# Optimization experiments

Measured on AMD Instinct MI355X. Metric: run time of the kernel, lower is better.

## Reference

```python
import jax, jax.numpy as jnp
import numpy as np

P = 8.0  # Lp norm order for NormDist layers (finite-p distance conv)
CHUNK = 8  # output-channel chunk for memory-bounded distance computation
EPS = 8.0 / 255.0


def lp_norm(d, p=P):
    # stable Lp norm over last axis: m * (sum((d/m)^p))^(1/p)
    m = jnp.max(d, axis=-1)
    ms = jnp.where(m > 0, m, 1.0)
    s = jnp.sum((d / ms[..., None]) ** p, axis=-1)
    ss = jnp.where(m > 0, s, 1.0)
    return m * ss ** (1.0 / p)


def extract_patches(t, k, s, pad):
    # [B,C,H,W] -> [B, L, C*k*k] (torch-unfold channel-major ordering), L=Ho*Wo
    pt = jax.lax.conv_general_dilated_patches(t, (k, k), (s, s), [(pad, pad), (pad, pad)])
    B, F, Ho, Wo = pt.shape
    return pt.reshape(B, F, Ho * Wo).transpose(0, 2, 1), Ho, Wo


def normdist_conv(c, lo, hi, w, k, s, pad):
    # Lp-distance conv with interval bound propagation on (center, lower, upper)
    pc, Ho, Wo = extract_patches(c, k, s, pad)
    pl, _, _ = extract_patches(lo, k, s, pad)
    ph, _, _ = extract_patches(hi, k, s, pad)
    O = w.shape[0]
    wf = w.reshape(O, -1)  # [O, F]

    def per_chunk(wc):  # wc: [CHUNK, F]
        dc = jnp.abs(pc[:, :, None, :] - wc)                     # [B,L,CHUNK,F]
        oc = lp_norm(dc)
        # per-element distance bounds given lo <= x <= hi
        dl = jnp.maximum(jnp.maximum(pl[:, :, None, :] - wc, wc - ph[:, :, None, :]), 0.0)
        ol = lp_norm(dl)
        dh = jnp.maximum(jnp.abs(pl[:, :, None, :] - wc), jnp.abs(ph[:, :, None, :] - wc))
        oh = lp_norm(dh)
        return oc, ol, oh

    oc, ol, oh = jax.lax.map(per_chunk, wf.reshape(O // CHUNK, CHUNK, -1))

    def to_img(t):  # [nch, B, L, CHUNK] -> [B, O, Ho, Wo]
        nch, B, L, ch = t.shape
        return t.transpose(1, 0, 3, 2).reshape(B, nch * ch, Ho, Wo)

    return to_img(oc), to_img(ol), to_img(oh)


def bound_relu(c, lo, hi):
    return jax.nn.relu(c), jax.nn.relu(lo), jax.nn.relu(hi)


def _mp(t):
    return jax.lax.reduce_window(t, -jnp.inf, jax.lax.max, (1, 1, 3, 3), (1, 1, 2, 2), 'VALID')


def bound_maxpool(c, lo, hi):
    return _mp(c), _mp(lo), _mp(hi)


def bound_linear(c, lo, hi, W, b=None):
    oc = c @ W.T
    mid = ((lo + hi) * 0.5) @ W.T
    rad = ((hi - lo) * 0.5) @ jnp.abs(W).T
    if b is not None:
        oc = oc + b
        mid = mid + b
    return oc, mid - rad, mid + rad


def setup_inputs() -> dict:
    key = jax.random.key(0)
    ks = jax.random.split(key, 10)
    x = jax.random.normal(ks[0], (16, 3, 32, 32), jnp.float32)
    lower = x - EPS
    upper = x + EPS
    w1 = jax.random.normal(ks[1], (96, 3, 7, 7), jnp.float32)
    w2 = jax.random.normal(ks[2], (256, 96, 5, 5), jnp.float32)
    w3 = jax.random.normal(ks[3], (384, 256, 3, 3), jnp.float32)
    w4 = jax.random.normal(ks[4], (384, 384, 3, 3), jnp.float32)
    w5 = jax.random.normal(ks[5], (256, 384, 3, 3), jnp.float32)
    fw1 = jax.random.normal(ks[6], (1024, 2304), jnp.float32) * 0.02
    fw2 = jax.random.normal(ks[7], (512, 1024), jnp.float32) * 0.03
    fw3 = jax.random.normal(ks[8], (10, 512), jnp.float32) * 0.04
    fb3 = jax.random.normal(ks[9], (10,), jnp.float32)
    return {"x": x, "lower": lower, "upper": upper, "w1": w1, "w2": w2, "w3": w3,
            "w4": w4, "w5": w5, "fw1": fw1, "fw2": fw2, "fw3": fw3, "fb3": fb3}


def reference(x, lower, upper, w1, w2, w3, w4, w5, fw1, fw2, fw3, fb3):
    c, l, u = normdist_conv(x, lower, upper, w1, 7, 2, 2)   # 32 -> 15
    c, l, u = bound_relu(c, l, u)
    c, l, u = bound_maxpool(c, l, u)                        # 15 -> 7
    c, l, u = normdist_conv(c, l, u, w2, 5, 1, 2)           # 7 -> 7
    c, l, u = bound_relu(c, l, u)
    c, l, u = bound_maxpool(c, l, u)                        # 7 -> 3
    c, l, u = normdist_conv(c, l, u, w3, 3, 1, 1)
    c, l, u = bound_relu(c, l, u)
    c, l, u = normdist_conv(c, l, u, w4, 3, 1, 1)
    c, l, u = bound_relu(c, l, u)
    c, l, u = normdist_conv(c, l, u, w5, 3, 1, 1)
    c, l, u = bound_relu(c, l, u)
    B = c.shape[0]
    c, l, u = c.reshape(B, -1), l.reshape(B, -1), u.reshape(B, -1)
    c, l, u = bound_linear(c, l, u, fw1)
    c, l, u = bound_relu(c, l, u)
    c, l, u = bound_linear(c, l, u, fw2)
    c, l, u = bound_relu(c, l, u)
    c, l, u = bound_linear(c, l, u, fw3, fb3)
    # final negation swaps the roles of lower/upper
    return (-c, -u, -l)
```

## Files before the change

kernel.cpp:

```cpp
#include <hip/hip_runtime.h>
#include <math.h>


__device__ __forceinline__ float rt8(float s) { return sqrtf(sqrtf(sqrtf(s))); }

__device__ __forceinline__ void tap16(float w, float pc, float pl, float pu,
                                      float& aC, float& aL, float& aH)
{
    float a = pc - w; float a2 = a * a, a4 = a2 * a2; aC = fmaf(a4, a4, aC);
    float x = pl - w, y = pu - w;
    float dl = fmaxf(fmaxf(x, -y), 0.f);
    float e2 = dl * dl, e4 = e2 * e2; aL = fmaf(e4, e4, aL);
    float h2 = fmaxf(x * x, y * y);
    float h4 = h2 * h2; aH = fmaf(h4, h4, aH);
}

__launch_bounds__(256)
__global__ void wtrans4(const float* __restrict__ W2, const float* __restrict__ W3,
                        const float* __restrict__ W4, const float* __restrict__ W5,
                        float* __restrict__ T2, float* __restrict__ T3,
                        float* __restrict__ T4, float* __restrict__ T5)
{
    constexpr int nt2 = 4 * 38, nt3 = 6 * 36, nt4 = 6 * 54, nt5 = 4 * 54;
    int bid = blockIdx.x;
    const float* W; float* T; int O, CK, t;
    if (bid < nt2)                   { W = W2; T = T2; O = 256; CK = 2400; t = bid; }
    else if (bid < nt2 + nt3)        { W = W3; T = T3; O = 384; CK = 2304; t = bid - nt2; }
    else if (bid < nt2 + nt3 + nt4)  { W = W4; T = T4; O = 384; CK = 3456; t = bid - nt2 - nt3; }
    else                             { W = W5; T = T5; O = 256; CK = 3456; t = bid - nt2 - nt3 - nt4; }
    int tilesC = (CK + 63) / 64;
    int to = t / tilesC, tc = t - to * tilesC;
    int o0 = to * 64, c0 = tc * 64;
    __shared__ float tile[64][65];
    int lane = threadIdx.x & 63, wv = threadIdx.x >> 6;
    #pragma unroll
    for (int i = 0; i < 16; ++i) {
        int row = wv + i * 4;
        int c = c0 + lane;
        tile[row][lane] = (c < CK) ? W[(size_t)(o0 + row) * CK + c] : 0.f;
    }
    __syncthreads();
    #pragma unroll
    for (int i = 0; i < 16; ++i) {
        int row = wv + i * 4;
        int c = c0 + row;
        if (c < CK) T[(size_t)c * O + o0 + lane] = tile[lane][row];
    }
}

template<int K, int S, int PAD, int CC, int HIN, int WIN, int HO, int WO>
__launch_bounds__(256)
__global__ void conv_a(const float* __restrict__ IC, const float* __restrict__ IL,
                       const float* __restrict__ IU, const float* __restrict__ W,
                       float* __restrict__ OUT, int B, int Cin, int O, int OG)
{
    constexpr int PH = (HO - 1) * S + K;
    constexpr int PW = (WO - 1) * S + K;
    constexpr int PP = PH * PW;
    constexpr int HW = HIN * WIN;
    constexpr int NP = HO * WO;
    constexpr int ROUNDS = (NP + 63) / 64;
    __shared__ float lds[CC * 3 * PP];

    int og = blockIdx.x % OG;
    int b  = (blockIdx.x / OG) % B;
    int tid = threadIdx.x;

    for (int i = tid; i < CC * 3 * PP; i += 256) lds[i] = 0.f;
    __syncthreads();
    for (int tsel = 0; tsel < 3; ++tsel) {
        const float* src = (tsel == 0 ? IC : (tsel == 1 ? IL : IU))
                         + (size_t)b * Cin * HW;
        for (int e = tid; e < CC * HW; e += 256) {
            int c = e / HW, p = e % HW;
            int pr = p / WIN, pw_ = p % WIN;
            lds[c * 3 * PP + tsel * PP + (pr + PAD) * PW + (pw_ + PAD)] = src[e];
        }
    }
    __syncthreads();

    int wave = tid >> 6, lane = tid & 63;
    int o = __builtin_amdgcn_readfirstlane(og * 4 + wave);
    const float* wp = W + (size_t)o * Cin * (K * K);

    for (int r = 0; r < ROUNDS; ++r) {
        int pos = r * 64 + lane;
        bool act = pos < NP;
        int pp = act ? pos : 0;
        int oh = pp / WO, ow = pp % WO;
        const float* sl = lds + (oh * S) * PW + ow * S;
        const float* wc = wp;
        float aC = 0.f, aL = 0.f, aH = 0.f;
        for (int c = 0; c < CC; ++c) {
            #pragma unroll
            for (int kh = 0; kh < K; ++kh)
                #pragma unroll
                for (int kw = 0; kw < K; ++kw) {
                    float w = wc[kh * K + kw];
                    tap16(w, sl[kh * PW + kw], sl[PP + kh * PW + kw],
                          sl[2 * PP + kh * PW + kw], aC, aL, aH);
                }
            sl += 3 * PP; wc += K * K;
        }
        if (act) {
            size_t N = (size_t)B * O * NP;
            size_t oidx = ((size_t)b * O + o) * NP + pos;
            OUT[oidx] = rt8(aC); OUT[N + oidx] = rt8(aL); OUT[2 * N + oidx] = rt8(aH);
        }
    }
}

template<int CC>
__launch_bounds__(256)
__global__ void conv2_kernel(const float* __restrict__ IN, const float* __restrict__ WT,
                             float* __restrict__ P, int nin)
{
    constexpr int B = 16, Cin = 96, O = 256;
    constexpr size_t N = (size_t)B * O * 49;
    __shared__ float slab[CC * 165];
    int x = blockIdx.x;
    int oh   = x % 7;
    int b    = (x / 7) % B;
    int chunk = x / (7 * B);
    int c0 = chunk * CC;
    int tid = threadIdx.x;

    for (int i = tid; i < CC * 165; i += 256) {
        int c = i / 165; int rem = i - c * 165;
        int tsel = rem / 55; int rr = rem - tsel * 55;
        int r = rr / 11, col = rr - r * 11;
        int ih = oh + r - 2, iw = col - 2;
        float v = 0.f;
        if ((unsigned)ih < 7u && (unsigned)iw < 7u)
            v = IN[(size_t)tsel * nin + ((size_t)b * Cin + c0 + c) * 49 + ih * 7 + iw];
        slab[i] = v;
    }
    __syncthreads();

    int o = tid;
    float aC[7], aL[7], aH[7];
    #pragma unroll
    for (int u = 0; u < 7; ++u) { aC[u] = 0.f; aL[u] = 0.f; aH[u] = 0.f; }

    for (int c = 0; c < CC; ++c) {
        const float* wp = WT + (size_t)((c0 + c) * 25) * O + o;
        float w[25];
        #pragma unroll
        for (int t = 0; t < 25; ++t) w[t] = wp[(size_t)t * O];
        const float* sb = slab + c * 165;
        #pragma unroll
        for (int r = 0; r < 5; ++r) {
            #pragma unroll
            for (int i = 0; i < 11; ++i) {
                float xc = sb[r * 11 + i];
                float xl = sb[55 + r * 11 + i];
                float xu = sb[110 + r * 11 + i];
                #pragma unroll
                for (int ow = 0; ow < 7; ++ow) {
                    int kw = i - ow;
                    if (kw >= 0 && kw < 5)
                        tap16(w[r * 5 + kw], xc, xl, xu, aC[ow], aL[ow], aH[ow]);
                }
            }
        }
    }

    float* Pc = P + (size_t)chunk * 3 * N;
    size_t rowbase = ((size_t)(b * 7 + oh) * 7) * O + o;
    #pragma unroll
    for (int u = 0; u < 7; ++u) {
        Pc[rowbase + (size_t)u * O]         = aC[u];
        Pc[N + rowbase + (size_t)u * O]     = aL[u];
        Pc[2 * N + rowbase + (size_t)u * O] = aH[u];
    }
}

__global__ void conv2_combine(const float* __restrict__ P, float* __restrict__ OUT, int NCH)
{
    constexpr int B = 16, O = 256;
    constexpr size_t N = (size_t)B * O * 49;
    size_t idx = (size_t)blockIdx.x * blockDim.x + threadIdx.x;
    if (idx >= 3 * N) return;
    float s = 0.f;
    for (int ch = 0; ch < NCH; ++ch) s += P[(size_t)ch * 3 * N + idx];
    size_t tsel = idx / N; size_t r = idx % N;
    int o = (int)(r % O); int pos = (int)((r / O) % 49); int b = (int)(r / (O * 49));
    OUT[tsel * N + ((size_t)b * O + o) * 49 + pos] = rt8(s);
}

template<int CC>
__launch_bounds__(384)
__global__ void conv3x3_kernel(const float* __restrict__ IN, const float* __restrict__ WT,
                               float* __restrict__ P, int nin, int B, int Cin, int O)
{
    __shared__ float slab[CC * 75];
    int x = blockIdx.x;
    int b = x % B;
    int chunk = x / B;
    int c0 = chunk * CC;
    int tid = threadIdx.x;

    for (int i = tid; i < CC * 75; i += blockDim.x) {
        int c = i / 75; int rem = i - c * 75;
        int tsel = rem / 25; int rr = rem - tsel * 25;
        int iy = rr / 5, ix = rr - iy * 5;
        int ih = iy - 1, iw = ix - 1;
        float v = 0.f;
        if ((unsigned)ih < 3u && (unsigned)iw < 3u)
            v = IN[(size_t)tsel * nin + ((size_t)b * Cin + c0 + c) * 9 + ih * 3 + iw];
        slab[i] = v;
    }
    __syncthreads();

    int o = tid;
    float aC[9], aL[9], aH[9];
    #pragma unroll
    for (int u = 0; u < 9; ++u) { aC[u] = 0.f; aL[u] = 0.f; aH[u] = 0.f; }

    for (int c = 0; c < CC; ++c) {
        const float* wp = WT + (size_t)((c0 + c) * 9) * O + o;
        float w[9];
        #pragma unroll
        for (int t = 0; t < 9; ++t) w[t] = wp[(size_t)t * O];
        const float* sb = slab + c * 75;
        #pragma unroll
        for (int iy = 0; iy < 5; ++iy) {
            #pragma unroll
            for (int ix = 0; ix < 5; ++ix) {
                float xc = sb[iy * 5 + ix];
                float xl = sb[25 + iy * 5 + ix];
                float xu = sb[50 + iy * 5 + ix];
                #pragma unroll
                for (int py = 0; py < 3; ++py) {
                    int ky = iy - py;
                    if (ky < 0 || ky > 2) continue;
                    #pragma unroll
                    for (int px = 0; px < 3; ++px) {
                        int kx = ix - px;
                        if (kx < 0 || kx > 2) continue;
                        tap16(w[ky * 3 + kx], xc, xl, xu,
                              aC[py * 3 + px], aL[py * 3 + px], aH[py * 3 + px]);
                    }
                }
            }
        }
    }

    size_t N = (size_t)B * O * 9;
    float* Pc = P + (size_t)chunk * 3 * N;
    size_t base = ((size_t)b * 9) * O + o;
    #pragma unroll
    for (int u = 0; u < 9; ++u) {
        Pc[base + (size_t)u * O]         = aC[u];
        Pc[N + base + (size_t)u * O]     = aL[u];
        Pc[2 * N + base + (size_t)u * O] = aH[u];
    }
}

__global__ void conv3_combine(const float* __restrict__ P, float* __restrict__ OUT,
                              int B, int O, int NCH)
{
    size_t N = (size_t)B * O * 9;
    size_t idx = (size_t)blockIdx.x * blockDim.x + threadIdx.x;
    if (idx >= 3 * N) return;
    float s = 0.f;
    for (int ch = 0; ch < NCH; ++ch) s += P[(size_t)ch * 3 * N + idx];
    size_t tsel = idx / N; size_t r = idx % N;
    int o = (int)(r % O); int pos = (int)((r / O) % 9); int b = (int)(r / ((size_t)O * 9));
    OUT[tsel * N + ((size_t)b * O + o) * 9 + pos] = rt8(s);
}

__global__ void maxpool_kernel(const float* __restrict__ in, float* __restrict__ out,
                               int BC, int Hin, int Win, int Ho, int Wo,
                               int n_in, int n_out)
{
    int idx = blockIdx.x * blockDim.x + threadIdx.x;
    int per = BC * Ho * Wo;
    if (idx >= 3 * per) return;
    int tsel = idx / per; int r = idx - tsel * per;
    int ow = r % Wo; int t2 = r / Wo;
    int oh = t2 % Ho; int bc = t2 / Ho;
    const float* ip = in + (size_t)tsel * n_in + (size_t)bc * Hin * Win;
    int ih0 = oh * 2, iw0 = ow * 2;
    float m = -INFINITY;
    #pragma unroll
    for (int i = 0; i < 3; ++i)
        #pragma unroll
        for (int j = 0; j < 3; ++j)
            m = fmaxf(m, ip[(ih0 + i) * Win + (iw0 + j)]);
    out[(size_t)tsel * n_out + r] = m;
}

__launch_bounds__(256)
__global__ void fc_gemv(const float* __restrict__ IC, const float* __restrict__ IL,
                        const float* __restrict__ IU, const float* __restrict__ W,
                        float* __restrict__ OUT, int B, int In, int Out)
{
    int gw = (int)((blockIdx.x * blockDim.x + threadIdx.x) >> 6);
    int lane = threadIdx.x & 63;
    if (gw >= B * Out) return;
    int o = gw % Out, b = gw / Out;
    const float4* wr = (const float4*)(W  + (size_t)o * In);
    const float4* cr = (const float4*)(IC + (size_t)b * In);
    const float4* lr = (const float4*)(IL + (size_t)b * In);
    const float4* ur = (const float4*)(IU + (size_t)b * In);
    int In4 = In >> 2;
    float sc = 0.f, sm = 0.f, sr = 0.f;
    for (int i = lane; i < In4; i += 64) {
        float4 w4 = wr[i], c4 = cr[i], l4 = lr[i], u4 = ur[i];
        sc = fmaf(c4.x, w4.x, sc); sc = fmaf(c4.y, w4.y, sc);
        sc = fmaf(c4.z, w4.z, sc); sc = fmaf(c4.w, w4.w, sc);
        sm = fmaf((l4.x + u4.x) * 0.5f, w4.x, sm);
        sm = fmaf((l4.y + u4.y) * 0.5f, w4.y, sm);
        sm = fmaf((l4.z + u4.z) * 0.5f, w4.z, sm);
        sm = fmaf((l4.w + u4.w) * 0.5f, w4.w, sm);
        sr = fmaf((u4.x - l4.x) * 0.5f, fabsf(w4.x), sr);
        sr = fmaf((u4.y - l4.y) * 0.5f, fabsf(w4.y), sr);
        sr = fmaf((u4.z - l4.z) * 0.5f, fabsf(w4.z), sr);
        sr = fmaf((u4.w - l4.w) * 0.5f, fabsf(w4.w), sr);
    }
    #pragma unroll
    for (int off = 32; off; off >>= 1) {
        sc += __shfl_xor(sc, off);
        sm += __shfl_xor(sm, off);
        sr += __shfl_xor(sr, off);
    }
    if (lane == 0) {
        size_t N = (size_t)B * Out;
        size_t idx = (size_t)b * Out + o;
        OUT[idx]         = fmaxf(sc, 0.f);
        OUT[N + idx]     = fmaxf(sm - sr, 0.f);
        OUT[2 * N + idx] = fmaxf(sm + sr, 0.f);
    }
}

__global__ void bound_linear_kernel(
    const float* __restrict__ IC, const float* __restrict__ IL, const float* __restrict__ IU,
    const float* __restrict__ W, const float* __restrict__ bias,
    float* __restrict__ OC, float* __restrict__ OL, float* __restrict__ OU,
    int B, int In, int Out)
{
    int idx = blockIdx.x * blockDim.x + threadIdx.x;
    if (idx >= B * Out) return;
    int o = idx % Out, b = idx / Out;
    const float* wr = W  + (size_t)o * In;
    const float* cr = IC + (size_t)b * In;
    const float* lr = IL + (size_t)b * In;
    const float* ur = IU + (size_t)b * In;
    float sc = 0.f, sm = 0.f, sr = 0.f;
    for (int i = 0; i < In; ++i) {
        float w = wr[i];
        sc = fmaf(cr[i], w, sc);
        sm = fmaf((lr[i] + ur[i]) * 0.5f, w, sm);
        sr = fmaf((ur[i] - lr[i]) * 0.5f, fabsf(w), sr);
    }
    float bb = bias[o]; sc += bb; sm += bb;
    OC[idx] = -sc; OL[idx] = -(sm - sr); OU[idx] = -(sm + sr);
}

extern "C" void kernel_launch(void* const* d_in, const int* in_sizes, int n_in,
                              void* d_out, int out_size, void* d_ws, size_t ws_size,
                              hipStream_t stream)
{
    const float* x   = (const float*)d_in[0];
    const float* lo  = (const float*)d_in[1];
    const float* hi  = (const float*)d_in[2];
    const float* w1  = (const float*)d_in[3];
    const float* w2  = (const float*)d_in[4];
    const float* w3  = (const float*)d_in[5];
    const float* w4  = (const float*)d_in[6];
    const float* w5  = (const float*)d_in[7];
    const float* fw1 = (const float*)d_in[8];
    const float* fw2 = (const float*)d_in[9];
    const float* fw3 = (const float*)d_in[10];
    const float* fb3 = (const float*)d_in[11];
    float* out = (float*)d_out;
    float* ws  = (float*)d_ws;

    const size_t n_c1 = 16u * 96 * 15 * 15;
    const size_t n_p1 = 16u * 96 * 7 * 7;
    const size_t n_c2 = 16u * 256 * 7 * 7;
    const size_t n_p2 = 16u * 256 * 3 * 3;
    const size_t n_c3 = 16u * 384 * 3 * 3;
    const size_t n_c4 = n_c3;
    const size_t n_c5 = 16u * 256 * 3 * 3;
    const size_t n_f1 = 16u * 1024;
    const size_t n_f2 = 16u * 512;

    float* A   = ws;
    float* Bp  = A  + 3 * n_c1;
    float* Cc  = Bp + 3 * n_p1;
    float* D   = Cc + 3 * n_c2;
    float* E   = D  + 3 * n_p2;
    float* F   = E  + 3 * n_c3;
    float* G   = F  + 3 * n_c4;
    float* H   = G  + 3 * n_c5;
    float* I   = H  + 3 * n_f1;
    float* WT2 = I  + 3 * n_f2;
    float* WT3 = WT2 + 614400;
    float* WT4 = WT3 + 884736;
    float* WT5 = WT4 + 1327104;
    float* SP  = WT5 + 884736;

    const int BS = 256;
    auto grid = [](size_t tot) { return dim3((unsigned)((tot + 255) / 256)); };

    wtrans4<<<4 * 38 + 6 * 36 + 6 * 54 + 4 * 54, BS, 0, stream>>>(
        w2, w3, w4, w5, WT2, WT3, WT4, WT5);

    conv_a<7, 2, 2, 3, 32, 32, 15, 15><<<384, BS, 0, stream>>>(
        x, lo, hi, w1, A, 16, 3, 96, 24);
    maxpool_kernel<<<grid(3 * n_p1), BS, 0, stream>>>(
        A, Bp, 16 * 96, 15, 15, 7, 7, (int)n_c1, (int)n_p1);
    conv2_kernel<6><<<16 * 16 * 7, 256, 0, stream>>>(Bp, WT2, SP, (int)n_p1);
    conv2_combine<<<grid(3 * n_c2), BS, 0, stream>>>(SP, Cc, 16);
    maxpool_kernel<<<grid(3 * n_p2), BS, 0, stream>>>(
        Cc, D, 16 * 256, 7, 7, 3, 3, (int)n_c2, (int)n_p2);
    conv3x3_kernel<8><<<32 * 16, 384, 0, stream>>>(
        D, WT3, SP, (int)n_p2, 16, 256, 384);
    conv3_combine<<<grid(3 * n_c3), BS, 0, stream>>>(SP, E, 16, 384, 32);
    conv3x3_kernel<8><<<48 * 16, 384, 0, stream>>>(
        E, WT4, SP, (int)n_c3, 16, 384, 384);
    conv3_combine<<<grid(3 * n_c4), BS, 0, stream>>>(SP, F, 16, 384, 48);
    conv3x3_kernel<8><<<48 * 16, 256, 0, stream>>>(
        F, WT5, SP, (int)n_c4, 16, 384, 256);
    conv3_combine<<<grid(3 * n_c5), BS, 0, stream>>>(SP, G, 16, 256, 48);
    fc_gemv<<<grid(16384u * 64), BS, 0, stream>>>(
        G, G + n_c5, G + 2 * n_c5, fw1, H, 16, 2304, 1024);
    fc_gemv<<<grid(8192u * 64), BS, 0, stream>>>(
        H, H + n_f1, H + 2 * n_f1, fw2, I, 16, 1024, 512);
    bound_linear_kernel<<<grid(160), BS, 0, stream>>>(
        I, I + n_f2, I + 2 * n_f2, fw3, fb3,
        out, out + 320, out + 160, 16, 512, 10);
}
```

Before: 670.1 us.

## Fuse conv2 combine with maxpool, keep channel-last intermediates, vectorize conv2 LDS reads

The 8th-root is moved after max-pooling, which is valid because the root is monotonic, so it runs on fewer elements. The conv2 partial-sum combine is fused with the following maxpool into one kernel. Intermediates between the 3x3 convs now stay in channel-last layout, so the combine becomes a flat sum and the transposing scatter is avoided. The conv2 slab is padded to 12 columns so its rows load as float4 vectors into registers, and the 3x3 tap loops are reordered to index outputs directly. The cost is strided gathers of input channels in conv3x3 slab loads, plus higher register pressure in conv2.

```diff
diff --git a/kernel.cpp b/kernel.cpp
--- a/kernel.cpp
+++ b/kernel.cpp
@@ -105,174 +105,14 @@
         if (act) {
             size_t N = (size_t)B * O * NP;
             size_t oidx = ((size_t)b * O + o) * NP + pos;
-            OUT[oidx] = rt8(aC); OUT[N + oidx] = rt8(aL); OUT[2 * N + oidx] = rt8(aH);
+            OUT[oidx] = aC; OUT[N + oidx] = aL; OUT[2 * N + oidx] = aH;
         }
     }
 }
 
-template<int CC>
-__launch_bounds__(256)
-__global__ void conv2_kernel(const float* __restrict__ IN, const float* __restrict__ WT,
-                             float* __restrict__ P, int nin)
-{
-    constexpr int B = 16, Cin = 96, O = 256;
-    constexpr size_t N = (size_t)B * O * 49;
-    __shared__ float slab[CC * 165];
-    int x = blockIdx.x;
-    int oh   = x % 7;
-    int b    = (x / 7) % B;
-    int chunk = x / (7 * B);
-    int c0 = chunk * CC;
-    int tid = threadIdx.x;
-
-    for (int i = tid; i < CC * 165; i += 256) {
-        int c = i / 165; int rem = i - c * 165;
-        int tsel = rem / 55; int rr = rem - tsel * 55;
-        int r = rr / 11, col = rr - r * 11;
-        int ih = oh + r - 2, iw = col - 2;
-        float v = 0.f;
-        if ((unsigned)ih < 7u && (unsigned)iw < 7u)
-            v = IN[(size_t)tsel * nin + ((size_t)b * Cin + c0 + c) * 49 + ih * 7 + iw];
-        slab[i] = v;
-    }
-    __syncthreads();
-
-    int o = tid;
-    float aC[7], aL[7], aH[7];
-    #pragma unroll
-    for (int u = 0; u < 7; ++u) { aC[u] = 0.f; aL[u] = 0.f; aH[u] = 0.f; }
-
-    for (int c = 0; c < CC; ++c) {
-        const float* wp = WT + (size_t)((c0 + c) * 25) * O + o;
-        float w[25];
-        #pragma unroll
-        for (int t = 0; t < 25; ++t) w[t] = wp[(size_t)t * O];
-        const float* sb = slab + c * 165;
-        #pragma unroll
-        for (int r = 0; r < 5; ++r) {
-            #pragma unroll
-            for (int i = 0; i < 11; ++i) {
-                float xc = sb[r * 11 + i];
-                float xl = sb[55 + r * 11 + i];
-                float xu = sb[110 + r * 11 + i];
-                #pragma unroll
-                for (int ow = 0; ow < 7; ++ow) {
-                    int kw = i - ow;
-                    if (kw >= 0 && kw < 5)
-                        tap16(w[r * 5 + kw], xc, xl, xu, aC[ow], aL[ow], aH[ow]);
-                }
-            }
-        }
-    }
-
-    float* Pc = P + (size_t)chunk * 3 * N;
-    size_t rowbase = ((size_t)(b * 7 + oh) * 7) * O + o;
-    #pragma unroll
-    for (int u = 0; u < 7; ++u) {
-        Pc[rowbase + (size_t)u * O]         = aC[u];
-        Pc[N + rowbase + (size_t)u * O]     = aL[u];
-        Pc[2 * N + rowbase + (size_t)u * O] = aH[u];
-    }
-}
-
-__global__ void conv2_combine(const float* __restrict__ P, float* __restrict__ OUT, int NCH)
-{
-    constexpr int B = 16, O = 256;
-    constexpr size_t N = (size_t)B * O * 49;
-    size_t idx = (size_t)blockIdx.x * blockDim.x + threadIdx.x;
-    if (idx >= 3 * N) return;
-    float s = 0.f;
-    for (int ch = 0; ch < NCH; ++ch) s += P[(size_t)ch * 3 * N + idx];
-    size_t tsel = idx / N; size_t r = idx % N;
-    int o = (int)(r % O); int pos = (int)((r / O) % 49); int b = (int)(r / (O * 49));
-    OUT[tsel * N + ((size_t)b * O + o) * 49 + pos] = rt8(s);
-}
-
-template<int CC>
-__launch_bounds__(384)
-__global__ void conv3x3_kernel(const float* __restrict__ IN, const float* __restrict__ WT,
-                               float* __restrict__ P, int nin, int B, int Cin, int O)
-{
-    __shared__ float slab[CC * 75];
-    int x = blockIdx.x;
-    int b = x % B;
-    int chunk = x / B;
-    int c0 = chunk * CC;
-    int tid = threadIdx.x;
-
-    for (int i = tid; i < CC * 75; i += blockDim.x) {
-        int c = i / 75; int rem = i - c * 75;
-        int tsel = rem / 25; int rr = rem - tsel * 25;
-        int iy = rr / 5, ix = rr - iy * 5;
-        int ih = iy - 1, iw = ix - 1;
-        float v = 0.f;
-        if ((unsigned)ih < 3u && (unsigned)iw < 3u)
-            v = IN[(size_t)tsel * nin + ((size_t)b * Cin + c0 + c) * 9 + ih * 3 + iw];
-        slab[i] = v;
-    }
-    __syncthreads();
-
-    int o = tid;
-    float aC[9], aL[9], aH[9];
-    #pragma unroll
-    for (int u = 0; u < 9; ++u) { aC[u] = 0.f; aL[u] = 0.f; aH[u] = 0.f; }
-
-    for (int c = 0; c < CC; ++c) {
-        const float* wp = WT + (size_t)((c0 + c) * 9) * O + o;
-        float w[9];
-        #pragma unroll
-        for (int t = 0; t < 9; ++t) w[t] = wp[(size_t)t * O];
-        const float* sb = slab + c * 75;
-        #pragma unroll
-        for (int iy = 0; iy < 5; ++iy) {
-            #pragma unroll
-            for (int ix = 0; ix < 5; ++ix) {
-                float xc = sb[iy * 5 + ix];
-                float xl = sb[25 + iy * 5 + ix];
-                float xu = sb[50 + iy * 5 + ix];
-                #pragma unroll
-                for (int py = 0; py < 3; ++py) {
-                    int ky = iy - py;
-                    if (ky < 0 || ky > 2) continue;
-                    #pragma unroll
-                    for (int px = 0; px < 3; ++px) {
-                        int kx = ix - px;
-                        if (kx < 0 || kx > 2) continue;
-                        tap16(w[ky * 3 + kx], xc, xl, xu,
-                              aC[py * 3 + px], aL[py * 3 + px], aH[py * 3 + px]);
-                    }
-                }
-            }
-        }
-    }
-
-    size_t N = (size_t)B * O * 9;
-    float* Pc = P + (size_t)chunk * 3 * N;
-    size_t base = ((size_t)b * 9) * O + o;
-    #pragma unroll
-    for (int u = 0; u < 9; ++u) {
-        Pc[base + (size_t)u * O]         = aC[u];
-        Pc[N + base + (size_t)u * O]     = aL[u];
-        Pc[2 * N + base + (size_t)u * O] = aH[u];
-    }
-}
-
-__global__ void conv3_combine(const float* __restrict__ P, float* __restrict__ OUT,
-                              int B, int O, int NCH)
-{
-    size_t N = (size_t)B * O * 9;
-    size_t idx = (size_t)blockIdx.x * blockDim.x + threadIdx.x;
-    if (idx >= 3 * N) return;
-    float s = 0.f;
-    for (int ch = 0; ch < NCH; ++ch) s += P[(size_t)ch * 3 * N + idx];
-    size_t tsel = idx / N; size_t r = idx % N;
-    int o = (int)(r % O); int pos = (int)((r / O) % 9); int b = (int)(r / ((size_t)O * 9));
-    OUT[tsel * N + ((size_t)b * O + o) * 9 + pos] = rt8(s);
-}
-
-__global__ void maxpool_kernel(const float* __restrict__ in, float* __restrict__ out,
-                               int BC, int Hin, int Win, int Ho, int Wo,
-                               int n_in, int n_out)
+__global__ void pool_rt8(const float* __restrict__ in, float* __restrict__ out,
+                         int BC, int Hin, int Win, int Ho, int Wo,
+                         int n_in, int n_out)
 {
     int idx = blockIdx.x * blockDim.x + threadIdx.x;
     int per = BC * Ho * Wo;
@@ -288,7 +128,183 @@
         #pragma unroll
         for (int j = 0; j < 3; ++j)
             m = fmaxf(m, ip[(ih0 + i) * Win + (iw0 + j)]);
-    out[(size_t)tsel * n_out + r] = m;
+    out[(size_t)tsel * n_out + r] = rt8(m);
+}
+
+template<int CC>
+__launch_bounds__(256)
+__global__ void conv2_kernel(const float* __restrict__ IN, const float* __restrict__ WT,
+                             float* __restrict__ P, int nin)
+{
+    constexpr int B = 16, Cin = 96, O = 256;
+    constexpr size_t N = (size_t)B * O * 49;
+    __shared__ __align__(16) float slab[CC * 180];
+    int x = blockIdx.x;
+    int oh   = x % 7;
+    int b    = (x / 7) % B;
+    int chunk = x / (7 * B);
+    int c0 = chunk * CC;
+    int tid = threadIdx.x;
+
+    for (int i = tid; i < CC * 180; i += 256) {
+        int c = i / 180; int rem = i - c * 180;
+        int tsel = rem / 60; int rr = rem - tsel * 60;
+        int r = rr / 12, col = rr - r * 12;
+        int ih = oh + r - 2, iw = col - 2;
+        float v = 0.f;
+        if (col < 11 && (unsigned)ih < 7u && (unsigned)iw < 7u)
+            v = IN[(size_t)tsel * nin + ((size_t)b * Cin + c0 + c) * 49 + ih * 7 + iw];
+        slab[i] = v;
+    }
+    __syncthreads();
+
+    int o = tid;
+    float aC[7], aL[7], aH[7];
+    #pragma unroll
+    for (int u = 0; u < 7; ++u) { aC[u] = 0.f; aL[u] = 0.f; aH[u] = 0.f; }
+
+    for (int c = 0; c < CC; ++c) {
+        const float* wp = WT + (size_t)((c0 + c) * 25) * O + o;
+        float w[25];
+        #pragma unroll
+        for (int t = 0; t < 25; ++t) w[t] = wp[(size_t)t * O];
+        const float* sb = slab + c * 180;
+        #pragma unroll
+        for (int r = 0; r < 5; ++r) {
+            float X[12], L[12], U[12];
+            const float4* px = (const float4*)(sb + r * 12);
+            const float4* pl = (const float4*)(sb + 60 + r * 12);
+            const float4* pu = (const float4*)(sb + 120 + r * 12);
+            ((float4*)X)[0] = px[0]; ((float4*)X)[1] = px[1]; ((float4*)X)[2] = px[2];
+            ((float4*)L)[0] = pl[0]; ((float4*)L)[1] = pl[1]; ((float4*)L)[2] = pl[2];
+            ((float4*)U)[0] = pu[0]; ((float4*)U)[1] = pu[1]; ((float4*)U)[2] = pu[2];
+            #pragma unroll
+            for (int ow = 0; ow < 7; ++ow)
+                #pragma unroll
+                for (int kw = 0; kw < 5; ++kw)
+                    tap16(w[r * 5 + kw], X[ow + kw], L[ow + kw], U[ow + kw],
+                          aC[ow], aL[ow], aH[ow]);
+        }
+    }
+
+    float* Pc = P + (size_t)chunk * 3 * N;
+    size_t rowbase = ((size_t)(b * 7 + oh) * 7) * O + o;
+    #pragma unroll
+    for (int u = 0; u < 7; ++u) {
+        Pc[rowbase + (size_t)u * O]         = aC[u];
+        Pc[N + rowbase + (size_t)u * O]     = aL[u];
+        Pc[2 * N + rowbase + (size_t)u * O] = aH[u];
+    }
+}
+
+__global__ void comb2_pool2(const float* __restrict__ P, float* __restrict__ D)
+{
+    constexpr int B = 16, O = 256, NCH = 16;
+    constexpr size_t N = (size_t)B * O * 49;
+    int idx = blockIdx.x * blockDim.x + threadIdx.x;
+    if (idx >= 3 * B * 9 * O) return;
+    int o = idx & 255; int t = idx >> 8;
+    int pos = t % 9; t /= 9;
+    int b = t % B; int tsel = t / B;
+    int ph = pos / 3, pw = pos % 3;
+    float m = 0.f;
+    #pragma unroll
+    for (int i = 0; i < 3; ++i)
+        #pragma unroll
+        for (int j = 0; j < 3; ++j) {
+            int sp = (ph * 2 + i) * 7 + (pw * 2 + j);
+            size_t base = (size_t)tsel * N + ((size_t)b * 49 + sp) * O + o;
+            float s = 0.f;
+            #pragma unroll
+            for (int ch = 0; ch < NCH; ++ch) s += P[(size_t)ch * 3 * N + base];
+            m = fmaxf(m, s);
+        }
+    D[idx] = rt8(m);
+}
+
+template<int CC>
+__launch_bounds__(384)
+__global__ void conv3x3_kernel(const float* __restrict__ IN, const float* __restrict__ WT,
+                               float* __restrict__ P, int B, int Cin, int O)
+{
+    __shared__ float slab[CC * 75];
+    int x = blockIdx.x;
+    int b = x % B;
+    int chunk = x / B;
+    int c0 = chunk * CC;
+    int tid = threadIdx.x;
+
+    for (int i = tid; i < CC * 75; i += blockDim.x) {
+        int c = i / 75; int rem = i - c * 75;
+        int tsel = rem / 25; int rr = rem - tsel * 25;
+        int iy = rr / 5, ix = rr - iy * 5;
+        int ih = iy - 1, iw = ix - 1;
+        float v = 0.f;
+        if ((unsigned)ih < 3u && (unsigned)iw < 3u)
+            v = IN[(((size_t)tsel * B + b) * 9 + (ih * 3 + iw)) * Cin + (c0 + c)];
+        slab[i] = v;
+    }
+    __syncthreads();
+
+    int o = tid;
+    float aC[9], aL[9], aH[9];
+    #pragma unroll
+    for (int u = 0; u < 9; ++u) { aC[u] = 0.f; aL[u] = 0.f; aH[u] = 0.f; }
+
+    for (int c = 0; c < CC; ++c) {
+        const float* wp = WT + (size_t)((c0 + c) * 9) * O + o;
+        float w[9];
+        #pragma unroll
+        for (int t = 0; t < 9; ++t) w[t] = wp[(size_t)t * O];
+        const float* sb = slab + c * 75;
+        #pragma unroll
+        for (int py = 0; py < 3; ++py)
+            #pragma unroll
+            for (int px = 0; px < 3; ++px)
+                #pragma unroll
+                for (int ky = 0; ky < 3; ++ky)
+                    #pragma unroll
+                    for (int kx = 0; kx < 3; ++kx) {
+                        int iy = py + ky, ix = px + kx;
+                        tap16(w[ky * 3 + kx], sb[iy * 5 + ix], sb[25 + iy * 5 + ix],
+                              sb[50 + iy * 5 + ix],
+                              aC[py * 3 + px], aL[py * 3 + px], aH[py * 3 + px]);
+                    }
+    }
+
+    size_t N = (size_t)B * O * 9;
+    float* Pc = P + (size_t)chunk * 3 * N;
+    size_t base = ((size_t)b * 9) * O + o;
+    #pragma unroll
+    for (int u = 0; u < 9; ++u) {
+        Pc[base + (size_t)u * O]         = aC[u];
+        Pc[N + base + (size_t)u * O]     = aL[u];
+        Pc[2 * N + base + (size_t)u * O] = aH[u];
+    }
+}
+
+__global__ void conv_comb_flat(const float* __restrict__ P, float* __restrict__ OUT,
+                               size_t N3, int NCH)
+{
+    size_t idx = (size_t)blockIdx.x * blockDim.x + threadIdx.x;
+    if (idx >= N3) return;
+    float s = 0.f;
+    for (int ch = 0; ch < NCH; ++ch) s += P[(size_t)ch * N3 + idx];
+    OUT[idx] = rt8(s);
+}
+
+__global__ void comb5_std(const float* __restrict__ P, float* __restrict__ G, int NCH)
+{
+    constexpr int B = 16, O = 256;
+    constexpr size_t N = (size_t)B * O * 9;
+    size_t idx = (size_t)blockIdx.x * blockDim.x + threadIdx.x;
+    if (idx >= 3 * N) return;
+    float s = 0.f;
+    for (int ch = 0; ch < NCH; ++ch) s += P[(size_t)ch * 3 * N + idx];
+    int o = (int)(idx % O); size_t t = idx / O;
+    int pos = (int)(t % 9); t /= 9;
+    int b = (int)(t % B); int tsel = (int)(t / B);
+    G[(size_t)tsel * N + ((size_t)b * O + o) * 9 + pos] = rt8(s);
 }
 
 __launch_bounds__(256)
@@ -379,21 +395,18 @@
 
     const size_t n_c1 = 16u * 96 * 15 * 15;
     const size_t n_p1 = 16u * 96 * 7 * 7;
-    const size_t n_c2 = 16u * 256 * 7 * 7;
-    const size_t n_p2 = 16u * 256 * 3 * 3;
-    const size_t n_c3 = 16u * 384 * 3 * 3;
-    const size_t n_c4 = n_c3;
-    const size_t n_c5 = 16u * 256 * 3 * 3;
+    const size_t n_d  = 16u * 256 * 9;
+    const size_t n_c3 = 16u * 384 * 9;
+    const size_t n_c5 = 16u * 256 * 9;
     const size_t n_f1 = 16u * 1024;
     const size_t n_f2 = 16u * 512;
 
     float* A   = ws;
     float* Bp  = A  + 3 * n_c1;
-    float* Cc  = Bp + 3 * n_p1;
-    float* D   = Cc + 3 * n_c2;
-    float* E   = D  + 3 * n_p2;
+    float* D   = Bp + 3 * n_p1;
+    float* E   = D  + 3 * n_d;
     float* F   = E  + 3 * n_c3;
-    float* G   = F  + 3 * n_c4;
+    float* G   = F  + 3 * n_c3;
     float* H   = G  + 3 * n_c5;
     float* I   = H  + 3 * n_f1;
     float* WT2 = I  + 3 * n_f2;
@@ -410,21 +423,16 @@
 
     conv_a<7, 2, 2, 3, 32, 32, 15, 15><<<384, BS, 0, stream>>>(
         x, lo, hi, w1, A, 16, 3, 96, 24);
-    maxpool_kernel<<<grid(3 * n_p1), BS, 0, stream>>>(
+    pool_rt8<<<grid(3 * n_p1), BS, 0, stream>>>(
         A, Bp, 16 * 96, 15, 15, 7, 7, (int)n_c1, (int)n_p1);
     conv2_kernel<6><<<16 * 16 * 7, 256, 0, stream>>>(Bp, WT2, SP, (int)n_p1);
-    conv2_combine<<<grid(3 * n_c2), BS, 0, stream>>>(SP, Cc, 16);
-    maxpool_kernel<<<grid(3 * n_p2), BS, 0, stream>>>(
-        Cc, D, 16 * 256, 7, 7, 3, 3, (int)n_c2, (int)n_p2);
-    conv3x3_kernel<8><<<32 * 16, 384, 0, stream>>>(
-        D, WT3, SP, (int)n_p2, 16, 256, 384);
-    conv3_combine<<<grid(3 * n_c3), BS, 0, stream>>>(SP, E, 16, 384, 32);
-    conv3x3_kernel<8><<<48 * 16, 384, 0, stream>>>(
-        E, WT4, SP, (int)n_c3, 16, 384, 384);
-    conv3_combine<<<grid(3 * n_c4), BS, 0, stream>>>(SP, F, 16, 384, 48);
-    conv3x3_kernel<8><<<48 * 16, 256, 0, stream>>>(
-        F, WT5, SP, (int)n_c4, 16, 384, 256);
-    conv3_combine<<<grid(3 * n_c5), BS, 0, stream>>>(SP, G, 16, 256, 48);
+    comb2_pool2<<<grid(3 * n_d), BS, 0, stream>>>(SP, D);
+    conv3x3_kernel<8><<<32 * 16, 384, 0, stream>>>(D, WT3, SP, 16, 256, 384);
+    conv_comb_flat<<<grid(3 * n_c3), BS, 0, stream>>>(SP, E, 3 * n_c3, 32);
+    conv3x3_kernel<8><<<48 * 16, 384, 0, stream>>>(E, WT4, SP, 16, 384, 384);
+    conv_comb_flat<<<grid(3 * n_c3), BS, 0, stream>>>(SP, F, 3 * n_c3, 48);
+    conv3x3_kernel<8><<<48 * 16, 256, 0, stream>>>(F, WT5, SP, 16, 384, 256);
+    comb5_std<<<grid(3 * n_c5), BS, 0, stream>>>(SP, G, 48);
     fc_gemv<<<grid(16384u * 64), BS, 0, stream>>>(
         G, G + n_c5, G + 2 * n_c5, fw1, H, 16, 2304, 1024);
     fc_gemv<<<grid(8192u * 64), BS, 0, stream>>>(
```

Measured after the change: 655.0 us. 2.3% less time.
